# Optimization experiments

Hardware: AMD Instinct MI355X
Metric: run time of the kernel (lower is better)

The kernel has to match this reference:

```python
import jax, jax.numpy as jnp
import numpy as np

B, N, F = 8, 16384, 32
S, K, OUT = 2048, 32, 128


def setup_inputs() -> dict:
    key = jax.random.key(0)
    k1, k2, k3, k4, k5, k6 = jax.random.split(key, 6)
    x = jax.random.normal(k1, (B, N, F), dtype=jnp.float32)
    # per-batch random subset of point indices (stand-in for randperm[:S])
    sample_idx = jax.random.randint(k2, (B, S), 0, N, dtype=jnp.int32)
    W1 = jax.random.normal(k3, (OUT, F), dtype=jnp.float32) * 0.1
    b1 = jax.random.normal(k4, (OUT,), dtype=jnp.float32) * 0.1
    W2 = jax.random.normal(k5, (OUT, OUT), dtype=jnp.float32) * 0.1
    b2 = jax.random.normal(k6, (OUT,), dtype=jnp.float32) * 0.1
    return {"x": x, "sample_idx": sample_idx, "W1": W1, "b1": b1, "W2": W2, "b2": b2}


def reference(x, sample_idx, W1, b1, W2, b2):
    # x: [B, N, F]; sample_idx: [B, S]
    sampled = jnp.take_along_axis(x, sample_idx[:, :, None], axis=1)  # [B, S, F]
    # squared euclidean distances in feature space: [B, S, N]
    x_sq = jnp.sum(x * x, axis=-1)                       # [B, N]
    s_sq = jnp.sum(sampled * sampled, axis=-1)           # [B, S]
    cross = jnp.einsum('bsf,bnf->bsn', sampled, x)       # [B, S, N]
    dist = s_sq[:, :, None] + x_sq[:, None, :] - 2.0 * cross
    # k nearest neighbors of each sampled point (includes itself)
    _, nbr_idx = jax.lax.top_k(-dist, K)                 # [B, S, K]
    # gather neighbor features: [B, S, K, F]
    groups = jnp.take_along_axis(x[:, None, :, :],
                                 nbr_idx[:, :, :, None], axis=2)
    # shared 1x1-conv MLP (two pointwise linears) + max-pool over neighbors
    h = jax.nn.relu(jnp.einsum('bskf,of->bsko', groups, W1) + b1)
    h = jnp.einsum('bsko,po->bskp', h, W2) + b2          # [B, S, K, OUT]
    features = jnp.max(h, axis=2)                        # [B, S, OUT]
    features_batch = jnp.transpose(features, (0, 2, 1))  # [B, OUT, S]
    sampled_batch = jnp.transpose(sampled, (0, 2, 1))    # [B, F, S]
    return (features_batch, sampled_batch)
```

## Files before the change

kernel.cpp:

```cpp
#include <hip/hip_runtime.h>
#include <math.h>

#pragma clang fp contract(off)

#define BB   8
#define NN   16384
#define FF   32
#define SS   2048
#define KK   32
#define OUTC 128

typedef float v2f __attribute__((ext_vector_type(2)));

__device__ __forceinline__ float uni(float v) {
    return __uint_as_float(__builtin_amdgcn_readfirstlane(__float_as_uint(v)));
}

__device__ __forceinline__ v2f splat2(float s) { v2f r; r.x = s; r.y = s; return r; }

__device__ __forceinline__ int mbcnt64(unsigned long long m) {
    return __builtin_amdgcn_mbcnt_hi((unsigned)(m >> 32),
           __builtin_amdgcn_mbcnt_lo((unsigned)m, 0));
}

__device__ __forceinline__ float np_sumsq32(const float* a) {
    float r[8];
#pragma unroll
    for (int j = 0; j < 8; j++) r[j] = a[j] * a[j];
#pragma unroll
    for (int t = 1; t < 4; t++) {
#pragma unroll
        for (int j = 0; j < 8; j++) {
            float e = a[8 * t + j] * a[8 * t + j];
            r[j] = r[j] + e;
        }
    }
    return ((r[0] + r[1]) + (r[2] + r[3])) + ((r[4] + r[5]) + (r[6] + r[7]));
}

__global__ __launch_bounds__(256) void xsq_kernel(const float* __restrict__ x,
                                                  float* __restrict__ xsq) {
    int gid = blockIdx.x * 256 + threadIdx.x;
    const float4* r = (const float4*)(x + (size_t)gid * FF);
    float a[32];
#pragma unroll
    for (int j = 0; j < 8; j++) {
        float4 v = r[j];
        a[4 * j] = v.x; a[4 * j + 1] = v.y; a[4 * j + 2] = v.z; a[4 * j + 3] = v.w;
    }
    xsq[gid] = np_sumsq32(a);
}

__global__ __launch_bounds__(256) void gather_kernel(const float* __restrict__ x,
                                                     const int* __restrict__ sidx,
                                                     float* __restrict__ sampled,
                                                     float* __restrict__ ssq) {
    int gid = blockIdx.x * 256 + threadIdx.x;
    int b = gid >> 11;
    int idx = sidx[gid];
    const float4* r = (const float4*)(x + ((size_t)b * NN + idx) * FF);
    float4* wo = (float4*)(sampled + (size_t)gid * FF);
    float a[32];
#pragma unroll
    for (int j = 0; j < 8; j++) {
        float4 v = r[j];
        a[4 * j] = v.x; a[4 * j + 1] = v.y; a[4 * j + 2] = v.z; a[4 * j + 3] = v.w;
        wo[j] = v;
    }
    ssq[gid] = np_sumsq32(a);
}

__global__ __launch_bounds__(256) void transpose_kernel(const float* __restrict__ sampled,
                                                        float* __restrict__ out_samp) {
    __shared__ float tile[32][65];
    int b = blockIdx.x >> 5, sg = blockIdx.x & 31;
    int s0 = sg * 64;
    int tid = threadIdx.x;
    int f = tid & 31, si = tid >> 5;
#pragma unroll
    for (int r = 0; r < 8; r++) {
        int s = r * 8 + si;
        tile[f][s] = sampled[((size_t)b * SS + s0 + s) * FF + f];
    }
    __syncthreads();
#pragma unroll
    for (int r = 0; r < 8; r++) {
        int flat = r * 256 + tid;
        int fo = flat >> 6, sw = flat & 63;
        out_samp[((size_t)b * FF + fo) * SS + s0 + sw] = tile[fo][sw];
    }
}

__global__ __launch_bounds__(256) void mlp_kernel(const float* __restrict__ x,
                                                  const float* __restrict__ W1,
                                                  const float* __restrict__ b1,
                                                  const float* __restrict__ W2,
                                                  const float* __restrict__ b2,
                                                  float* __restrict__ h2) {
    __shared__ float xs[64][36];
    __shared__ float hs[8512];
    int tid = threadIdx.x, lane = tid & 63;
    int wu = __builtin_amdgcn_readfirstlane(tid >> 6);
    size_t p0 = (size_t)blockIdx.x * 64;

    for (int i = tid; i < 64 * 8; i += 256) {
        int row = i >> 3, seg = i & 7;
        *(float4*)&xs[row][seg * 4] = *(const float4*)(x + (p0 + row) * FF + seg * 4);
    }
    __syncthreads();

    float xr[32];
    {
        const float4* r = (const float4*)&xs[lane][0];
#pragma unroll
        for (int j = 0; j < 8; j++) {
            float4 v = r[j];
            xr[4 * j] = v.x; xr[4 * j + 1] = v.y; xr[4 * j + 2] = v.z; xr[4 * j + 3] = v.w;
        }
    }
#pragma unroll 4
    for (int i = 0; i < 32; i++) {
        int o = wu * 32 + i;
        const float4* wr = (const float4*)(W1 + o * FF);
        float a = b1[o];
#pragma unroll
        for (int j = 0; j < 8; j++) {
            float4 v = wr[j];
            a = fmaf(v.x, xr[4 * j], a);     a = fmaf(v.y, xr[4 * j + 1], a);
            a = fmaf(v.z, xr[4 * j + 2], a); a = fmaf(v.w, xr[4 * j + 3], a);
        }
        hs[o * 65 + lane] = fmaxf(a, 0.f);
    }
    __syncthreads();
    float acc[32];
#pragma unroll
    for (int i = 0; i < 32; i++) acc[i] = b2[wu * 32 + i];
    for (int k4 = 0; k4 < 32; k4++) {
        float h0 = hs[(4 * k4 + 0) * 65 + lane];
        float h1v = hs[(4 * k4 + 1) * 65 + lane];
        float h2v = hs[(4 * k4 + 2) * 65 + lane];
        float h3v = hs[(4 * k4 + 3) * 65 + lane];
#pragma unroll
        for (int i = 0; i < 32; i++) {
            const float4 v = *(const float4*)(W2 + (wu * 32 + i) * OUTC + 4 * k4);
            acc[i] = fmaf(v.x, h0, acc[i]);  acc[i] = fmaf(v.y, h1v, acc[i]);
            acc[i] = fmaf(v.z, h2v, acc[i]); acc[i] = fmaf(v.w, h3v, acc[i]);
        }
    }
    __syncthreads();
#pragma unroll 4
    for (int i = 0; i < 32; i++) hs[lane * 133 + wu * 32 + i] = acc[i];
    __syncthreads();
    for (int j = 0; j < 32; j++) {
        int flat = j * 256 + tid;
        int p = flat >> 7, o = flat & 127;
        h2[(p0 + p) * OUTC + o] = hs[p * 133 + o];
    }
}

__device__ __forceinline__ bool lessp(float da, int ia, float db, int ib) {
    return da < db || (da == db && ia < ib);
}
__device__ __forceinline__ void cswap(float& d, int& i, int j, bool dirAsc, int lane) {
    float od = __shfl_xor(d, j);
    int   oi = __shfl_xor(i, j);
    bool lower = (lane & j) == 0;
    bool oLess = lessp(od, oi, d, i);
    if (oLess == (lower == dirAsc)) { d = od; i = oi; }
}
__device__ __forceinline__ void sort64(float& d, int& i, bool asc, int lane) {
#pragma unroll
    for (int k = 2; k <= 64; k <<= 1) {
        bool ba = (((lane & k) == 0) == asc);
#pragma unroll
        for (int j = k >> 1; j > 0; j >>= 1) cswap(d, i, j, ba, lane);
    }
}
__device__ __forceinline__ float wave_compact2(float* bd, int* bi, int m, int lane) {
    float d0 = (lane < m) ? bd[lane] : INFINITY;
    int   i0 = (lane < m) ? bi[lane] : 0x7fffffff;
    float d1 = (lane + 64 < m) ? bd[lane + 64] : INFINITY;
    int   i1 = (lane + 64 < m) ? bi[lane + 64] : 0x7fffffff;
    sort64(d0, i0, true, lane);
    sort64(d1, i1, false, lane);
    bool t = lessp(d1, i1, d0, i0);
    float ld = t ? d1 : d0;
    int   li = t ? i1 : i0;
#pragma unroll
    for (int j = 32; j > 0; j >>= 1) cswap(ld, li, j, true, lane);
    bd[lane] = ld; bi[lane] = li;
    return uni(__shfl(ld, 31));
}

__global__ __launch_bounds__(256, 6) void topk_kernel(const float* __restrict__ x,
                                                      const float* __restrict__ x_sq,
                                                      const float* __restrict__ sampled,
                                                      const float* __restrict__ s_sq,
                                                      int* __restrict__ nbr) {
    int b = blockIdx.x & 7;
    int qg = blockIdx.x >> 3;
    int tid = threadIdx.x, lane = tid & 63;
    int w = __builtin_amdgcn_readfirstlane(tid >> 6);
    __shared__ float xs[64][36];
    __shared__ float bufd[8][128];
    __shared__ int   bufi[8][128];
    int s0 = qg * 8;
    const float* xb = x + (size_t)b * (NN * FF);
    const float* xqb = x_sq + (size_t)b * NN;

    v2f qp[32];
    {
        const float* sp0 = sampled + ((size_t)b * SS + s0 + w * 2 + 0) * FF;
        const float* sp1 = sampled + ((size_t)b * SS + s0 + w * 2 + 1) * FF;
#pragma unroll
        for (int k = 0; k < 32; k++) {
            qp[k].x = uni(sp0[k]);
            qp[k].y = uni(sp1[k]);
        }
    }
    v2f ssq01;
    ssq01.x = uni(s_sq[b * SS + s0 + w * 2 + 0]);
    ssq01.y = uni(s_sq[b * SS + s0 + w * 2 + 1]);

    float* bq0d = &bufd[w * 2 + 0][0];  int* bq0i = &bufi[w * 2 + 0][0];
    float* bq1d = &bufd[w * 2 + 1][0];  int* bq1i = &bufi[w * 2 + 1][0];
    int   cnt0 = 0, cnt1 = 0;
    float tau0 = INFINITY, tau1 = INFINITY;

    int r0 = tid >> 3, c0 = (tid & 7) * 4;
    const float4* g0 = (const float4*)(xb + (size_t)r0 * FF + c0);
    const float4* g1 = (const float4*)(xb + (size_t)(r0 + 32) * FF + c0);
    float4 p0 = g0[0], p1 = g1[0];
    float xq = xqb[lane];

    for (int t = 0; t < NN / 64; t++) {
        *(float4*)&xs[r0][c0] = p0;
        *(float4*)&xs[r0 + 32][c0] = p1;
        if (t + 1 < NN / 64) {
            p0 = g0[(size_t)(t + 1) * 512];
            p1 = g1[(size_t)(t + 1) * 512];
        }
        __syncthreads();
        int n = t * 64 + lane;
        float xq_c = xq;
        v2f c01; c01.x = 0.f; c01.y = 0.f;
        {
            const float4* rr = (const float4*)&xs[lane][0];
#pragma unroll
            for (int j = 0; j < 8; j++) {
                float4 v = rr[j];
                c01 = __builtin_elementwise_fma(qp[4 * j + 0], splat2(v.x), c01);
                c01 = __builtin_elementwise_fma(qp[4 * j + 1], splat2(v.y), c01);
                c01 = __builtin_elementwise_fma(qp[4 * j + 2], splat2(v.z), c01);
                c01 = __builtin_elementwise_fma(qp[4 * j + 3], splat2(v.w), c01);
            }
        }
        if (t + 1 < NN / 64) xq = xqb[(t + 1) * 64 + lane];

        v2f d01 = (ssq01 + splat2(xq_c)) - (c01 + c01);
        float d0v = d01.x;
        float d1v = d01.y;

        unsigned long long m0 = __ballot(d0v < tau0);
        if (m0) {
            int pos = cnt0 + mbcnt64(m0);
            if (d0v < tau0) { bq0d[pos] = d0v; bq0i[pos] = n; }
            cnt0 += __builtin_popcountll(m0);
            if (cnt0 > 64) { tau0 = wave_compact2(bq0d, bq0i, cnt0, lane); cnt0 = 32; }
        }
        unsigned long long m1 = __ballot(d1v < tau1);
        if (m1) {
            int pos = cnt1 + mbcnt64(m1);
            if (d1v < tau1) { bq1d[pos] = d1v; bq1i[pos] = n; }
            cnt1 += __builtin_popcountll(m1);
            if (cnt1 > 64) { tau1 = wave_compact2(bq1d, bq1i, cnt1, lane); cnt1 = 32; }
        }
        __syncthreads();
    }
    wave_compact2(bq0d, bq0i, cnt0, lane);
    wave_compact2(bq1d, bq1i, cnt1, lane);
    int s = s0 + w * 2;
    if (lane < 32) {
        nbr[((size_t)b * SS + s) * KK + lane] = bq0i[lane];
        nbr[((size_t)b * SS + s + 1) * KK + lane] = bq1i[lane];
    }
}

__global__ __launch_bounds__(128) void maxgather_kernel(const float* __restrict__ h2,
                                                        const int* __restrict__ nbr,
                                                        float* __restrict__ out_feat) {
    __shared__ float fs[128][17];
    int b = blockIdx.x & 7;
    int sg = blockIdx.x >> 3;
    int s0 = sg * 16;
    int tid = threadIdx.x;
    for (int si = 0; si < 16; si++) {
        int s = s0 + si;
        const int* row = nbr + ((size_t)b * SS + s) * KK;
        float m = -INFINITY;
#pragma unroll 4
        for (int k = 0; k < KK; k++) {
            int idx = row[k];
            float v = h2[((size_t)b * NN + idx) * OUTC + tid];
            m = fmaxf(m, v);
        }
        fs[tid][si] = m;
    }
    __syncthreads();
#pragma unroll
    for (int j = 0; j < 16; j++) {
        int flat = j * 128 + tid;
        int fo = flat >> 4, sw = flat & 15;
        out_feat[((size_t)b * OUTC + fo) * SS + s0 + sw] = fs[fo][sw];
    }
}

extern "C" void kernel_launch(void* const* d_in, const int* in_sizes, int n_in,
                              void* d_out, int out_size, void* d_ws, size_t ws_size,
                              hipStream_t stream) {
    const float* x    = (const float*)d_in[0];
    const int*   sidx = (const int*)d_in[1];
    const float* W1   = (const float*)d_in[2];
    const float* b1   = (const float*)d_in[3];
    const float* W2   = (const float*)d_in[4];
    const float* b2   = (const float*)d_in[5];

    float* out_feat = (float*)d_out;
    float* out_samp = out_feat + (size_t)BB * OUTC * SS;

    float* h2      = (float*)d_ws;
    float* sampled = h2 + (size_t)BB * NN * OUTC;
    float* xsq     = sampled + (size_t)BB * SS * FF;
    float* ssq     = xsq + (size_t)BB * NN;
    int*   nbr     = (int*)(ssq + (size_t)BB * SS);

    xsq_kernel<<<dim3(BB * NN / 256), dim3(256), 0, stream>>>(x, xsq);
    gather_kernel<<<dim3(BB * SS / 256), dim3(256), 0, stream>>>(x, sidx, sampled, ssq);
    mlp_kernel<<<dim3(BB * NN / 64), dim3(256), 0, stream>>>(x, W1, b1, W2, b2, h2);
    transpose_kernel<<<dim3(BB * SS / 64), dim3(256), 0, stream>>>(sampled, out_samp);
    topk_kernel<<<dim3(BB * SS / 8), dim3(256), 0, stream>>>(x, xsq, sampled, ssq, nbr);
    maxgather_kernel<<<dim3(BB * SS / 16), dim3(128), 0, stream>>>(h2, nbr, out_feat);
}
```

Baseline: 1.035 ms.

## Load point tiles directly into registers with double buffering, dropping LDS staging

The top-k kernel no longer stages each 64-point tile of x through shared memory with block-wide barriers. Each lane now loads its own point's 32 features straight from global memory into registers, ping-ponging between two register buffers to prefetch the next tile. This removes the two __syncthreads per tile and the LDS round trip. In exchange the four waves of a block each fetch the same tile redundantly, relying on L1/L2. Register use rises, so the launch-bounds occupancy hint drops from 6 to 4.

Result: slower. 2.143 ms (+107.1%).

```diff
diff --git a/kernel.cpp b/kernel.cpp
--- a/kernel.cpp
+++ b/kernel.cpp
@@ -192,7 +192,37 @@
     return uni(__shfl(ld, 31));
 }
 
-__global__ __launch_bounds__(256, 6) void topk_kernel(const float* __restrict__ x,
+__device__ __forceinline__ void insert_cand(float dv, int n, int lane,
+                                            float* bd, int* bi, int& cnt, float& tau) {
+    unsigned long long m = __ballot(dv < tau);
+    if (m) {
+        int pos = cnt + mbcnt64(m);
+        if (dv < tau) { bd[pos] = dv; bi[pos] = n; }
+        cnt += __builtin_popcountll(m);
+        if (cnt > 64) { tau = wave_compact2(bd, bi, cnt, lane); cnt = 32; }
+    }
+}
+
+__device__ __forceinline__ void tile_pass(const float4* buf, int t, float xq, int lane,
+                                          const v2f* qp, v2f ssq01,
+                                          float* bq0d, int* bq0i, int& cnt0, float& tau0,
+                                          float* bq1d, int* bq1i, int& cnt1, float& tau1) {
+    v2f c01; c01.x = 0.f; c01.y = 0.f;
+#pragma unroll
+    for (int j = 0; j < 8; j++) {
+        float4 v = buf[j];
+        c01 = __builtin_elementwise_fma(qp[4 * j + 0], splat2(v.x), c01);
+        c01 = __builtin_elementwise_fma(qp[4 * j + 1], splat2(v.y), c01);
+        c01 = __builtin_elementwise_fma(qp[4 * j + 2], splat2(v.z), c01);
+        c01 = __builtin_elementwise_fma(qp[4 * j + 3], splat2(v.w), c01);
+    }
+    v2f d01 = (ssq01 + splat2(xq)) - (c01 + c01);
+    int n = t * 64 + lane;
+    insert_cand(d01.x, n, lane, bq0d, bq0i, cnt0, tau0);
+    insert_cand(d01.y, n, lane, bq1d, bq1i, cnt1, tau1);
+}
+
+__global__ __launch_bounds__(256, 4) void topk_kernel(const float* __restrict__ x,
                                                       const float* __restrict__ x_sq,
                                                       const float* __restrict__ sampled,
                                                       const float* __restrict__ s_sq,
@@ -201,7 +231,6 @@
     int qg = blockIdx.x >> 3;
     int tid = threadIdx.x, lane = tid & 63;
     int w = __builtin_amdgcn_readfirstlane(tid >> 6);
-    __shared__ float xs[64][36];
     __shared__ float bufd[8][128];
     __shared__ int   bufi[8][128];
     int s0 = qg * 8;
@@ -227,55 +256,29 @@
     int   cnt0 = 0, cnt1 = 0;
     float tau0 = INFINITY, tau1 = INFINITY;
 
-    int r0 = tid >> 3, c0 = (tid & 7) * 4;
-    const float4* g0 = (const float4*)(xb + (size_t)r0 * FF + c0);
-    const float4* g1 = (const float4*)(xb + (size_t)(r0 + 32) * FF + c0);
-    float4 p0 = g0[0], p1 = g1[0];
-    float xq = xqb[lane];
-
-    for (int t = 0; t < NN / 64; t++) {
-        *(float4*)&xs[r0][c0] = p0;
-        *(float4*)&xs[r0 + 32][c0] = p1;
-        if (t + 1 < NN / 64) {
-            p0 = g0[(size_t)(t + 1) * 512];
-            p1 = g1[(size_t)(t + 1) * 512];
-        }
-        __syncthreads();
-        int n = t * 64 + lane;
-        float xq_c = xq;
-        v2f c01; c01.x = 0.f; c01.y = 0.f;
-        {
-            const float4* rr = (const float4*)&xs[lane][0];
-#pragma unroll
-            for (int j = 0; j < 8; j++) {
-                float4 v = rr[j];
-                c01 = __builtin_elementwise_fma(qp[4 * j + 0], splat2(v.x), c01);
-                c01 = __builtin_elementwise_fma(qp[4 * j + 1], splat2(v.y), c01);
-                c01 = __builtin_elementwise_fma(qp[4 * j + 2], splat2(v.z), c01);
-                c01 = __builtin_elementwise_fma(qp[4 * j + 3], splat2(v.w), c01);
-            }
-        }
-        if (t + 1 < NN / 64) xq = xqb[(t + 1) * 64 + lane];
-
-        v2f d01 = (ssq01 + splat2(xq_c)) - (c01 + c01);
-        float d0v = d01.x;
-        float d1v = d01.y;
-
-        unsigned long long m0 = __ballot(d0v < tau0);
-        if (m0) {
-            int pos = cnt0 + mbcnt64(m0);
-            if (d0v < tau0) { bq0d[pos] = d0v; bq0i[pos] = n; }
-            cnt0 += __builtin_popcountll(m0);
-            if (cnt0 > 64) { tau0 = wave_compact2(bq0d, bq0i, cnt0, lane); cnt0 = 32; }
-        }
-        unsigned long long m1 = __ballot(d1v < tau1);
-        if (m1) {
-            int pos = cnt1 + mbcnt64(m1);
-            if (d1v < tau1) { bq1d[pos] = d1v; bq1i[pos] = n; }
-            cnt1 += __builtin_popcountll(m1);
-            if (cnt1 > 64) { tau1 = wave_compact2(bq1d, bq1i, cnt1, lane); cnt1 = 32; }
-        }
-        __syncthreads();
+    const float4* lp = (const float4*)xb + (size_t)lane * 8;
+    float4 bufA[8], bufB[8];
+    float xqA, xqB;
+#pragma unroll
+    for (int j = 0; j < 8; j++) bufA[j] = lp[j];
+    xqA = xqb[lane];
+
+    for (int t = 0; t < NN / 64; t += 2) {
+#pragma unroll
+        for (int j = 0; j < 8; j++) bufB[j] = lp[(size_t)(t + 1) * 512 + j];
+        xqB = xqb[(t + 1) * 64 + lane];
+
+        tile_pass(bufA, t, xqA, lane, qp, ssq01,
+                  bq0d, bq0i, cnt0, tau0, bq1d, bq1i, cnt1, tau1);
+
+        if (t + 2 < NN / 64) {
+#pragma unroll
+            for (int j = 0; j < 8; j++) bufA[j] = lp[(size_t)(t + 2) * 512 + j];
+            xqA = xqb[(t + 2) * 64 + lane];
+        }
+
+        tile_pass(bufB, t + 1, xqB, lane, qp, ssq01,
+                  bq0d, bq0i, cnt0, tau0, bq1d, bq1i, cnt1, tau1);
     }
     wave_compact2(bq0d, bq0i, cnt0, lane);
     wave_compact2(bq1d, bq1i, cnt1, lane);
```

## Process four queries per wave in top-k kernel to reuse LDS tiles

Applied to the files above, without the earlier changes.

Each wave of the top-k kernel now handles four sampled query points instead of two, so every block covers 16 queries and the grid shrinks by half. Each LDS tile of x is read once per lane and reused for twice as many dot products. This halves the global and LDS traffic for x per query and interleaves two independent FMA chains. The cost is higher register pressure: the second query pair is kept in per-lane VGPRs, not scalars, and occupancy is lowered to 4 blocks per CU. There are also fewer blocks in flight and more serial candidate-insertion work per wave.

Measured after the change: 1.146 ms. +10.7%, slower.

```diff
diff --git a/kernel.cpp b/kernel.cpp
--- a/kernel.cpp
+++ b/kernel.cpp
@@ -192,7 +192,18 @@
     return uni(__shfl(ld, 31));
 }
 
-__global__ __launch_bounds__(256, 6) void topk_kernel(const float* __restrict__ x,
+__device__ __forceinline__ void insert_cand(float dv, int n, int lane,
+                                            float* bd, int* bi, int& cnt, float& tau) {
+    unsigned long long m = __ballot(dv < tau);
+    if (m) {
+        int pos = cnt + mbcnt64(m);
+        if (dv < tau) { bd[pos] = dv; bi[pos] = n; }
+        cnt += __builtin_popcountll(m);
+        if (cnt > 64) { tau = wave_compact2(bd, bi, cnt, lane); cnt = 32; }
+    }
+}
+
+__global__ __launch_bounds__(256, 4) void topk_kernel(const float* __restrict__ x,
                                                       const float* __restrict__ x_sq,
                                                       const float* __restrict__ sampled,
                                                       const float* __restrict__ s_sq,
@@ -202,30 +213,38 @@
     int tid = threadIdx.x, lane = tid & 63;
     int w = __builtin_amdgcn_readfirstlane(tid >> 6);
     __shared__ float xs[64][36];
-    __shared__ float bufd[8][128];
-    __shared__ int   bufi[8][128];
-    int s0 = qg * 8;
+    __shared__ float bufd[16][128];
+    __shared__ int   bufi[16][128];
+    int s0 = qg * 16;
     const float* xb = x + (size_t)b * (NN * FF);
     const float* xqb = x_sq + (size_t)b * NN;
 
-    v2f qp[32];
+    v2f qpA[32], qpB[32];
     {
-        const float* sp0 = sampled + ((size_t)b * SS + s0 + w * 2 + 0) * FF;
-        const float* sp1 = sampled + ((size_t)b * SS + s0 + w * 2 + 1) * FF;
+        const float* sp0 = sampled + ((size_t)b * SS + s0 + w * 4 + 0) * FF;
+        const float* sp1 = sampled + ((size_t)b * SS + s0 + w * 4 + 1) * FF;
+        const float* sp2 = sampled + ((size_t)b * SS + s0 + w * 4 + 2) * FF;
+        const float* sp3 = sampled + ((size_t)b * SS + s0 + w * 4 + 3) * FF;
 #pragma unroll
         for (int k = 0; k < 32; k++) {
-            qp[k].x = uni(sp0[k]);
-            qp[k].y = uni(sp1[k]);
-        }
-    }
-    v2f ssq01;
-    ssq01.x = uni(s_sq[b * SS + s0 + w * 2 + 0]);
-    ssq01.y = uni(s_sq[b * SS + s0 + w * 2 + 1]);
-
-    float* bq0d = &bufd[w * 2 + 0][0];  int* bq0i = &bufi[w * 2 + 0][0];
-    float* bq1d = &bufd[w * 2 + 1][0];  int* bq1i = &bufi[w * 2 + 1][0];
-    int   cnt0 = 0, cnt1 = 0;
-    float tau0 = INFINITY, tau1 = INFINITY;
+            qpA[k].x = uni(sp0[k]);
+            qpA[k].y = uni(sp1[k]);
+            qpB[k].x = sp2[k];
+            qpB[k].y = sp3[k];
+        }
+    }
+    v2f ssqA, ssqB;
+    ssqA.x = uni(s_sq[b * SS + s0 + w * 4 + 0]);
+    ssqA.y = uni(s_sq[b * SS + s0 + w * 4 + 1]);
+    ssqB.x = s_sq[b * SS + s0 + w * 4 + 2];
+    ssqB.y = s_sq[b * SS + s0 + w * 4 + 3];
+
+    float* bq0d = &bufd[w * 4 + 0][0];  int* bq0i = &bufi[w * 4 + 0][0];
+    float* bq1d = &bufd[w * 4 + 1][0];  int* bq1i = &bufi[w * 4 + 1][0];
+    float* bq2d = &bufd[w * 4 + 2][0];  int* bq2i = &bufi[w * 4 + 2][0];
+    float* bq3d = &bufd[w * 4 + 3][0];  int* bq3i = &bufi[w * 4 + 3][0];
+    int   cnt0 = 0, cnt1 = 0, cnt2 = 0, cnt3 = 0;
+    float tau0 = INFINITY, tau1 = INFINITY, tau2 = INFINITY, tau3 = INFINITY;
 
     int r0 = tid >> 3, c0 = (tid & 7) * 4;
     const float4* g0 = (const float4*)(xb + (size_t)r0 * FF + c0);
@@ -241,48 +260,45 @@
             p1 = g1[(size_t)(t + 1) * 512];
         }
         __syncthreads();
-        int n = t * 64 + lane;
         float xq_c = xq;
-        v2f c01; c01.x = 0.f; c01.y = 0.f;
+        if (t + 1 < NN / 64) xq = xqb[(t + 1) * 64 + lane];
+
+        v2f cA; cA.x = 0.f; cA.y = 0.f;
+        v2f cB; cB.x = 0.f; cB.y = 0.f;
         {
             const float4* rr = (const float4*)&xs[lane][0];
 #pragma unroll
             for (int j = 0; j < 8; j++) {
                 float4 v = rr[j];
-                c01 = __builtin_elementwise_fma(qp[4 * j + 0], splat2(v.x), c01);
-                c01 = __builtin_elementwise_fma(qp[4 * j + 1], splat2(v.y), c01);
-                c01 = __builtin_elementwise_fma(qp[4 * j + 2], splat2(v.z), c01);
-                c01 = __builtin_elementwise_fma(qp[4 * j + 3], splat2(v.w), c01);
+                cA = __builtin_elementwise_fma(qpA[4 * j + 0], splat2(v.x), cA);
+                cB = __builtin_elementwise_fma(qpB[4 * j + 0], splat2(v.x), cB);
+                cA = __builtin_elementwise_fma(qpA[4 * j + 1], splat2(v.y), cA);
+                cB = __builtin_elementwise_fma(qpB[4 * j + 1], splat2(v.y), cB);
+                cA = __builtin_elementwise_fma(qpA[4 * j + 2], splat2(v.z), cA);
+                cB = __builtin_elementwise_fma(qpB[4 * j + 2], splat2(v.z), cB);
+                cA = __builtin_elementwise_fma(qpA[4 * j + 3], splat2(v.w), cA);
+                cB = __builtin_elementwise_fma(qpB[4 * j + 3], splat2(v.w), cB);
             }
         }
-        if (t + 1 < NN / 64) xq = xqb[(t + 1) * 64 + lane];
-
-        v2f d01 = (ssq01 + splat2(xq_c)) - (c01 + c01);
-        float d0v = d01.x;
-        float d1v = d01.y;
-
-        unsigned long long m0 = __ballot(d0v < tau0);
-        if (m0) {
-            int pos = cnt0 + mbcnt64(m0);
-            if (d0v < tau0) { bq0d[pos] = d0v; bq0i[pos] = n; }
-            cnt0 += __builtin_popcountll(m0);
-            if (cnt0 > 64) { tau0 = wave_compact2(bq0d, bq0i, cnt0, lane); cnt0 = 32; }
-        }
-        unsigned long long m1 = __ballot(d1v < tau1);
-        if (m1) {
-            int pos = cnt1 + mbcnt64(m1);
-            if (d1v < tau1) { bq1d[pos] = d1v; bq1i[pos] = n; }
-            cnt1 += __builtin_popcountll(m1);
-            if (cnt1 > 64) { tau1 = wave_compact2(bq1d, bq1i, cnt1, lane); cnt1 = 32; }
-        }
+        v2f dA = (ssqA + splat2(xq_c)) - (cA + cA);
+        v2f dB = (ssqB + splat2(xq_c)) - (cB + cB);
+        int n = t * 64 + lane;
+        insert_cand(dA.x, n, lane, bq0d, bq0i, cnt0, tau0);
+        insert_cand(dA.y, n, lane, bq1d, bq1i, cnt1, tau1);
+        insert_cand(dB.x, n, lane, bq2d, bq2i, cnt2, tau2);
+        insert_cand(dB.y, n, lane, bq3d, bq3i, cnt3, tau3);
         __syncthreads();
     }
     wave_compact2(bq0d, bq0i, cnt0, lane);
     wave_compact2(bq1d, bq1i, cnt1, lane);
-    int s = s0 + w * 2;
+    wave_compact2(bq2d, bq2i, cnt2, lane);
+    wave_compact2(bq3d, bq3i, cnt3, lane);
+    int s = s0 + w * 4;
     if (lane < 32) {
-        nbr[((size_t)b * SS + s) * KK + lane] = bq0i[lane];
+        nbr[((size_t)b * SS + s) * KK + lane]     = bq0i[lane];
         nbr[((size_t)b * SS + s + 1) * KK + lane] = bq1i[lane];
+        nbr[((size_t)b * SS + s + 2) * KK + lane] = bq2i[lane];
+        nbr[((size_t)b * SS + s + 3) * KK + lane] = bq3i[lane];
     }
 }
 
@@ -338,6 +354,6 @@
     gather_kernel<<<dim3(BB * SS / 256), dim3(256), 0, stream>>>(x, sidx, sampled, ssq);
     mlp_kernel<<<dim3(BB * NN / 64), dim3(256), 0, stream>>>(x, W1, b1, W2, b2, h2);
     transpose_kernel<<<dim3(BB * SS / 64), dim3(256), 0, stream>>>(sampled, out_samp);
-    topk_kernel<<<dim3(BB * SS / 8), dim3(256), 0, stream>>>(x, xsq, sampled, ssq, nbr);
+    topk_kernel<<<dim3(BB * SS / 16), dim3(256), 0, stream>>>(x, xsq, sampled, ssq, nbr);
     maxgather_kernel<<<dim3(BB * SS / 16), dim3(128), 0, stream>>>(h2, nbr, out_feat);
 }
```
